# Optimization experiments

Hardware: AMD Instinct MI355X
Metric: run time of the kernel (lower is better)

Reference implementation:

```python
import jax, jax.numpy as jnp
import numpy as np

N_NODES = 100000
N_EDGES = 500000
D = 128
D_OUT = 128


def setup_inputs() -> dict:
    key = jax.random.key(0)
    k1, k2, k3, k4, k5 = jax.random.split(key, 5)
    x = jax.random.normal(k1, (N_NODES, D), dtype=jnp.float32)
    pos_edge_index = jax.random.randint(k2, (2, N_EDGES), 0, N_NODES, dtype=jnp.int64)
    neg_edge_index = jax.random.randint(k3, (2, N_EDGES), 0, N_NODES, dtype=jnp.int64)
    W = jax.random.normal(k4, (3 * D, D_OUT), dtype=jnp.float32) * (1.0 / np.sqrt(3 * D))
    b = jax.random.normal(k5, (D_OUT,), dtype=jnp.float32) * 0.01
    return {"x": x, "pos_edge_index": pos_edge_index, "neg_edge_index": neg_edge_index, "W": W, "b": b}


def _agg(x, edge_index):
    # PyG add-aggregation: message x_j gathered from source (row 0),
    # scatter-added to destination (row 1).
    src, dst = edge_index[0], edge_index[1]
    return jax.ops.segment_sum(x[src], dst, num_segments=x.shape[0])


def reference(x, pos_edge_index, neg_edge_index, W, b):
    x_pos = _agg(x, pos_edge_index)  # [N, D]
    x_neg = _agg(x, neg_edge_index)  # [N, D]
    out_cat = jnp.concatenate((x, x_pos, x_neg), axis=1)  # [N, 3D]
    return out_cat @ W + b  # [N, D_OUT]
```

## Files before the change

### kernel.cpp

```cpp
#include <hip/hip_runtime.h>

#define NNODES 100000
#define NEDGES 500000
#define DD 128
#define NBUK 1563
#define BCAP 896
#define BINB 123
#define ZBYTE ((unsigned int)NNODES << 8)

typedef __attribute__((ext_vector_type(8))) short short8v;
typedef __attribute__((ext_vector_type(4))) float f32x4;

__device__ __forceinline__ unsigned short f2bf(float f) {
    unsigned int u = __float_as_uint(f);
    return (unsigned short)((u + 0x7FFFu + ((u >> 16) & 1u)) >> 16);
}
__device__ __forceinline__ unsigned int f2bf2(float a, float b) {
    return (unsigned int)f2bf(a) | ((unsigned int)f2bf(b) << 16);
}
__device__ __forceinline__ float bflo(unsigned int v) {
    return __uint_as_float(v << 16);
}
__device__ __forceinline__ float bfhi(unsigned int v) {
    return __uint_as_float(v & 0xFFFF0000u);
}

__global__ __launch_bounds__(256) void init_kernel(
        int* __restrict__ gcur, const unsigned int* __restrict__ e,
        int* __restrict__ flag) {
    if (blockIdx.x < 7) {
        const int i = blockIdx.x * 256 + threadIdx.x;
        if (i < NBUK) gcur[i] = 0;
        return;
    }
    __shared__ unsigned int s_acc;
    if (threadIdx.x == 0) s_acc = 0u;
    __syncthreads();
    unsigned int v = 0u;
    for (int i = threadIdx.x; i < 4096; i += 256)
        v |= e[2 * i + 1];
    for (int off = 32; off > 0; off >>= 1)
        v |= __shfl_down(v, off, 64);
    if ((threadIdx.x & 63) == 0) atomicOr(&s_acc, v);
    __syncthreads();
    if (threadIdx.x == 0) *flag = (s_acc == 0u) ? 1 : 0;
}

__global__ __launch_bounds__(256) void prep_kernel(
        const float4* __restrict__ x4, uint2* __restrict__ xb2,
        const float* __restrict__ W, unsigned short* __restrict__ wb,
        const void* __restrict__ pe, const void* __restrict__ ne,
        const int* __restrict__ flag,
        int* __restrict__ gcur, unsigned int* __restrict__ regions) {
    const int b = blockIdx.x;
    if (b < BINB) {
        __shared__ int hist[NBUK];
        __shared__ int gbase[NBUK];
        const int tid = threadIdx.x;
        for (int i = tid; i < NBUK; i += 256) hist[i] = 0;
        __syncthreads();
        const int e0 = b * 8192;
        const int fl = *flag;
        for (int k0 = 0; k0 < 32; k0 += 8) {
            int dv[8];
            bool ok[8];
#pragma unroll
            for (int j = 0; j < 8; ++j) {
                const int i = e0 + (k0 + j) * 256 + tid;
                ok[j] = i < 2 * NEDGES;
                const int ic = ok[j] ? i : 0;
                const int list = ic >= NEDGES;
                const int e = ic - list * NEDGES;
                const void* ed = list ? ne : pe;
                dv[j] = fl ? (int)((const long long*)ed)[NEDGES + e]
                           : ((const int*)ed)[NEDGES + e];
            }
#pragma unroll
            for (int j = 0; j < 8; ++j)
                if (ok[j]) atomicAdd(&hist[dv[j] >> 6], 1);
        }
        __syncthreads();
        for (int i = tid; i < NBUK; i += 256) {
            const int h = hist[i];
            gbase[i] = h ? atomicAdd(&gcur[i], h) : 0;
            hist[i] = 0;
        }
        __syncthreads();
        for (int k0 = 0; k0 < 32; k0 += 8) {
            unsigned int ent[8];
            int bk[8];
            bool ok[8];
#pragma unroll
            for (int j = 0; j < 8; ++j) {
                const int i = e0 + (k0 + j) * 256 + tid;
                ok[j] = i < 2 * NEDGES;
                const int ic = ok[j] ? i : 0;
                const int list = ic >= NEDGES;
                const int e = ic - list * NEDGES;
                int s, d;
                if (fl) {
                    const long long* p = (const long long*)(list ? ne : pe);
                    s = (int)p[e]; d = (int)p[NEDGES + e];
                } else {
                    const int* p = (const int*)(list ? ne : pe);
                    s = p[e]; d = p[NEDGES + e];
                }
                bk[j] = d >> 6;
                ent[j] = ((unsigned int)s << 7) |
                         ((unsigned int)(d & 63) << 1) | (unsigned int)list;
            }
            int pos[8];
#pragma unroll
            for (int j = 0; j < 8; ++j)
                if (ok[j]) pos[j] = gbase[bk[j]] + atomicAdd(&hist[bk[j]], 1);
#pragma unroll
            for (int j = 0; j < 8; ++j)
                if (ok[j] && pos[j] < BCAP)
                    regions[(size_t)bk[j] * BCAP + pos[j]] = ent[j];
        }
    } else if (b < BINB + 24) {
        const int t = (b - BINB) * 256 + threadIdx.x;
        const int l = t & 63;
        const int nf = (t >> 6) & 7;
        const int s = t >> 9;
        const int n = nf * 16 + (l & 15);
        const int k0 = s * 32 + (l >> 4) * 8;
        unsigned short* o = wb + (size_t)t * 8;
#pragma unroll
        for (int j = 0; j < 8; ++j)
            o[j] = f2bf(W[(size_t)(k0 + j) * DD + n]);
    } else if (b == BINB + 24) {
        if (threadIdx.x < 64)
            ((unsigned int*)xb2)[(size_t)NNODES * 64 + threadIdx.x] = 0u;
    } else {
        const int n = NNODES * DD / 4;
        for (int i = (b - BINB - 25) * 256 + threadIdx.x; i < n; i += 512 * 256) {
            const float4 v = x4[i];
            uint2 o;
            o.x = f2bf2(v.x, v.y);
            o.y = f2bf2(v.z, v.w);
            xb2[i] = o;
        }
    }
}

__global__ __launch_bounds__(512) void aggemm_kernel(
        const char* __restrict__ xbb,
        const int* __restrict__ gcur, const unsigned int* __restrict__ regions,
        const unsigned short* __restrict__ wb,
        const float* __restrict__ bias,
        float* __restrict__ out) {
    __shared__ unsigned short tile[64 * 264];
    __shared__ unsigned int sorted[BCAP];
    __shared__ int cnt[128];
    __shared__ int tmp[128];
    __shared__ int sstart[129];
    __shared__ int scur[128];

    const int b = blockIdx.x;
    const int node0 = b * 64;
    const int tid = threadIdx.x;
    const int wid = tid >> 6;
    const int lane = tid & 63;

    int n = gcur[b];
    n = n < BCAP ? n : BCAP;
    const unsigned int* __restrict__ reg = regions + (size_t)b * BCAP;

    if (tid < 128) cnt[tid] = 0;
    __syncthreads();
    for (int i = tid; i < n; i += 512)
        atomicAdd(&cnt[reg[i] & 127u], 1);
    __syncthreads();
    if (tid < 128) tmp[tid] = cnt[tid];
    __syncthreads();
#pragma unroll
    for (int off = 1; off < 128; off <<= 1) {
        int v = 0;
        if (tid < 128 && tid >= off) v = tmp[tid - off];
        __syncthreads();
        if (tid < 128) tmp[tid] += v;
        __syncthreads();
    }
    if (tid < 128) {
        const int st = tmp[tid] - cnt[tid];
        sstart[tid] = st;
        scur[tid] = st;
    }
    if (tid == 127) sstart[128] = tmp[127];
    __syncthreads();
    for (int i = tid; i < n; i += 512) {
        const unsigned int ent = reg[i];
        const int pos = atomicAdd(&scur[ent & 127u], 1);
        sorted[pos] = ((ent >> 7) << 8) | (ent & 127u);
    }
    __syncthreads();

    const int lm = lane & 15;
    const int lk = lane >> 4;
    const int rg = wid & 3;
    const int ch = wid >> 2;
    const int rl0 = rg * 16;
    int rowg = node0 + rl0 + lm;
    if (rowg > NNODES) rowg = NNODES;
    const unsigned short* __restrict__ xb = (const unsigned short*)xbb;
    short8v a0pre[4];
#pragma unroll
    for (int s = 0; s < 4; ++s)
        a0pre[s] = *(const short8v*)(xb + (size_t)rowg * 128 + s * 32 + lk * 8);

    unsigned int* tileW = (unsigned int*)tile;
#pragma unroll
    for (int r = 0; r < 8; ++r) {
        tileW[(wid * 8 + r) * 132 + lane] = 0u;
        tileW[(wid * 8 + r) * 132 + 64 + lane] = 0u;
    }
    const int lo = sstart[wid * 16];
    const int hi = sstart[wid * 16 + 16];
    const unsigned int lane4 = lane * 4;
    unsigned int cur = 255u;
    float ax = 0.f, ay = 0.f;
    for (int base = lo; base < hi; base += 8) {
        unsigned int ent[8];
#pragma unroll
        for (int j = 0; j < 8; ++j) {
            const int ii = base + j;
            ent[j] = (ii < hi) ? sorted[ii] : (ZBYTE | 255u);
        }
        unsigned int v[8];
#pragma unroll
        for (int j = 0; j < 8; ++j)
            v[j] = *(const unsigned int*)(
                xbb + (size_t)((ent[j] & 0xFFFFFF00u) + lane4));
#pragma unroll
        for (int j = 0; j < 8; ++j) {
            const unsigned int s = ent[j] & 255u;
            if (s != cur) {
                if (cur != 255u) {
                    unsigned int* w =
                        &tileW[(cur >> 1) * 132 + (cur & 1) * 64 + lane];
                    const unsigned int o = *w;
                    *w = f2bf2(bflo(o) + ax, bfhi(o) + ay);
                }
                cur = s;
                ax = 0.f;
                ay = 0.f;
            }
            ax += bflo(v[j]);
            ay += bfhi(v[j]);
        }
    }
    if (cur != 255u) {
        unsigned int* w = &tileW[(cur >> 1) * 132 + (cur & 1) * 64 + lane];
        const unsigned int o = *w;
        *w = f2bf2(bflo(o) + ax, bfhi(o) + ay);
    }
    __syncthreads();

    f32x4 acc[4];
#pragma unroll
    for (int nf = 0; nf < 4; ++nf) acc[nf] = (f32x4)(0.f);

    for (int c = 0; c < 3; ++c) {
#pragma unroll
        for (int s = 0; s < 4; ++s) {
            short8v a;
            if (c == 0)
                a = a0pre[s];
            else
                a = *(const short8v*)(tile + (rl0 + lm) * 264 +
                                      (c - 1) * 128 + s * 32 + lk * 8);
            const short8v* __restrict__ bp =
                (const short8v*)wb + ((size_t)((c * 4 + s) * 8 + ch * 4)) * 64 + lane;
#pragma unroll
            for (int nf = 0; nf < 4; ++nf)
                acc[nf] = __builtin_amdgcn_mfma_f32_16x16x32_bf16(
                    a, bp[nf * 64], acc[nf], 0, 0, 0);
        }
    }

    const int rbase = node0 + rl0 + lk * 4;
#pragma unroll
    for (int nf = 0; nf < 4; ++nf) {
        const int col = (ch * 4 + nf) * 16 + lm;
        const float bv = bias[col];
#pragma unroll
        for (int r = 0; r < 4; ++r) {
            const int row = rbase + r;
            if (row < NNODES)
                out[(size_t)row * 128 + col] = acc[nf][r] + bv;
        }
    }
}

extern "C" void kernel_launch(void* const* d_in, const int* in_sizes, int n_in,
                              void* d_out, int out_size, void* d_ws, size_t ws_size,
                              hipStream_t stream) {
    const float* x     = (const float*)d_in[0];
    const void*  pos_e = d_in[1];
    const void*  neg_e = d_in[2];
    const float* W     = (const float*)d_in[3];
    const float* bias  = (const float*)d_in[4];
    float*       out   = (float*)d_out;

    const size_t XB = ((size_t)NNODES + 1) * DD * 2;
    const size_t WB = 12 * 8 * 64 * 8 * 2;
    const size_t GB = 8192;
    const size_t RB = (size_t)NBUK * BCAP * 4;

    char* ws = (char*)d_ws;
    int* flag = (int*)ws;
    size_t off = 256;
    unsigned int*   xb      = (unsigned int*)(ws + off);   off += XB;
    unsigned short* wb      = (unsigned short*)(ws + off); off += WB;
    int*            gcur    = (int*)(ws + off);            off += GB;
    unsigned int*   regions = (unsigned int*)(ws + off);   off += RB;
    (void)ws_size;

    init_kernel<<<8, 256, 0, stream>>>(gcur, (const unsigned int*)pos_e, flag);

    prep_kernel<<<BINB + 25 + 512, 256, 0, stream>>>(
        (const float4*)x, (uint2*)xb, W, wb, pos_e, neg_e, flag, gcur, regions);

    aggemm_kernel<<<NBUK, 512, 0, stream>>>(
        (const char*)xb, gcur, regions, wb, bias, out);
}
```

Measured before the change: 100.1 us.

## Gather two edges per wave with 8-byte loads and cross-half shuffle reduction

Pads each destination segment's edge list to an even length with a zero-row sentinel. Each wave then splits into two 32-lane halves that gather alternate edges using 8-byte loads instead of 4-byte loads, which halves the number of gather instructions per edge. Partial sums from the two halves are combined with a cross-half shuffle before being written as bf16 into the shared tile. Segment flushes now overwrite instead of read-modify-write, which relies on each segment being processed as one contiguous run. The costs are extra shuffles per flush, padding loads of the zero row, and a larger sorted buffer.

```diff
diff --git a/kernel.cpp b/kernel.cpp
--- a/kernel.cpp
+++ b/kernel.cpp
@@ -151,7 +151,7 @@
         const float* __restrict__ bias,
         float* __restrict__ out) {
     __shared__ unsigned short tile[64 * 264];
-    __shared__ unsigned int sorted[BCAP];
+    __shared__ unsigned int sorted[1024];
     __shared__ int cnt[128];
     __shared__ int tmp[128];
     __shared__ int sstart[129];
@@ -172,7 +172,7 @@
     for (int i = tid; i < n; i += 512)
         atomicAdd(&cnt[reg[i] & 127u], 1);
     __syncthreads();
-    if (tid < 128) tmp[tid] = cnt[tid];
+    if (tid < 128) tmp[tid] = cnt[tid] + (cnt[tid] & 1);
     __syncthreads();
 #pragma unroll
     for (int off = 1; off < 128; off <<= 1) {
@@ -183,7 +183,8 @@
         __syncthreads();
     }
     if (tid < 128) {
-        const int st = tmp[tid] - cnt[tid];
+        const int pc = cnt[tid] + (cnt[tid] & 1);
+        const int st = tmp[tid] - pc;
         sstart[tid] = st;
         scur[tid] = st;
     }
@@ -194,6 +195,9 @@
         const int pos = atomicAdd(&scur[ent & 127u], 1);
         sorted[pos] = ((ent >> 7) << 8) | (ent & 127u);
     }
+    __syncthreads();
+    if (tid < 128 && (cnt[tid] & 1))
+        sorted[sstart[tid] + cnt[tid]] = ZBYTE | (unsigned int)tid;
     __syncthreads();
 
     const int lm = lane & 15;
@@ -215,46 +219,54 @@
         tileW[(wid * 8 + r) * 132 + lane] = 0u;
         tileW[(wid * 8 + r) * 132 + 64 + lane] = 0u;
     }
+    __syncthreads();
     const int lo = sstart[wid * 16];
     const int hi = sstart[wid * 16 + 16];
-    const unsigned int lane4 = lane * 4;
+    const int half = lane >> 5;
+    const unsigned int lane8 = (lane & 31) * 8;
     unsigned int cur = 255u;
-    float ax = 0.f, ay = 0.f;
-    for (int base = lo; base < hi; base += 8) {
+    float c0 = 0.f, c1 = 0.f, c2 = 0.f, c3 = 0.f;
+
+#define FLUSH(SEG)                                                            \
+    do {                                                                      \
+        const float r0 = __shfl_xor(c0, 32, 64);                              \
+        const float r1 = __shfl_xor(c1, 32, 64);                              \
+        const float r2 = __shfl_xor(c2, 32, 64);                              \
+        const float r3 = __shfl_xor(c3, 32, 64);                              \
+        const float ta = half ? (c2 + r2) : (c0 + r0);                        \
+        const float tb = half ? (c3 + r3) : (c1 + r1);                        \
+        tileW[((SEG) >> 1) * 132 + ((SEG) & 1) * 64 + (lane & 31) * 2 + half] \
+            = f2bf2(ta, tb);                                                  \
+    } while (0)
+
+    for (int base = lo; base < hi; base += 16) {
         unsigned int ent[8];
 #pragma unroll
         for (int j = 0; j < 8; ++j) {
-            const int ii = base + j;
+            const int ii = base + j * 2 + half;
             ent[j] = (ii < hi) ? sorted[ii] : (ZBYTE | 255u);
         }
-        unsigned int v[8];
+        uint2 v[8];
 #pragma unroll
         for (int j = 0; j < 8; ++j)
-            v[j] = *(const unsigned int*)(
-                xbb + (size_t)((ent[j] & 0xFFFFFF00u) + lane4));
+            v[j] = *(const uint2*)(
+                xbb + (size_t)((ent[j] & 0xFFFFFF00u) + lane8));
 #pragma unroll
         for (int j = 0; j < 8; ++j) {
             const unsigned int s = ent[j] & 255u;
             if (s != cur) {
-                if (cur != 255u) {
-                    unsigned int* w =
-                        &tileW[(cur >> 1) * 132 + (cur & 1) * 64 + lane];
-                    const unsigned int o = *w;
-                    *w = f2bf2(bflo(o) + ax, bfhi(o) + ay);
-                }
+                if (cur != 255u) FLUSH(cur);
                 cur = s;
-                ax = 0.f;
-                ay = 0.f;
+                c0 = 0.f; c1 = 0.f; c2 = 0.f; c3 = 0.f;
             }
-            ax += bflo(v[j]);
-            ay += bfhi(v[j]);
-        }
-    }
-    if (cur != 255u) {
-        unsigned int* w = &tileW[(cur >> 1) * 132 + (cur & 1) * 64 + lane];
-        const unsigned int o = *w;
-        *w = f2bf2(bflo(o) + ax, bfhi(o) + ay);
-    }
+            c0 += bflo(v[j].x);
+            c1 += bfhi(v[j].x);
+            c2 += bflo(v[j].y);
+            c3 += bfhi(v[j].y);
+        }
+    }
+    if (cur != 255u) FLUSH(cur);
+#undef FLUSH
     __syncthreads();
 
     f32x4 acc[4];
```

Result: slower. 102.6 us (+2.5%).
